# Performance work log

Hardware: AMD Instinct MI355X
Metric: run time of the kernel (lower is better)

Reference implementation:

```python
import jax, jax.numpy as jnp
import numpy as np

BLOCK = 16  # NVFP4 block size (one fp8e4m3 scale per 16 elements)
FP4_LEVELS = jnp.array([0.0, 0.5, 1.0, 1.5, 2.0, 3.0, 4.0, 6.0], dtype=jnp.float32)  # e2m1 magnitudes
FP4_MIDS = jnp.array([0.25, 0.75, 1.25, 1.75, 2.5, 3.5, 5.0], dtype=jnp.float32)     # round-to-nearest midpoints
FP8_MIN = 2.0 ** -9   # smallest positive fp8e4m3 subnormal (guards div-by-zero after scale cast)
FP8_MAX = 448.0


def fp8_e4m3_round(x):
    """Emulate casting positive float32 values to fp8 e4m3 (3 mantissa bits)."""
    e = jnp.clip(jnp.floor(jnp.log2(jnp.maximum(x, 1e-30))), -6.0, 8.0)  # -6 = min normal exponent
    step = jnp.exp2(e - 3.0)
    return jnp.clip(jnp.round(x / step) * step, 0.0, FP8_MAX)


def fp4_e2m1_quant(x):
    """Round-to-nearest onto the signed fp4 e2m1 grid {0,±0.5,±1,±1.5,±2,±3,±4,±6}."""
    idx = jnp.sum(jnp.abs(x)[..., None] > FP4_MIDS, axis=-1)
    return jnp.sign(x) * FP4_LEVELS[idx]


def quantize_activations(x2):
    """x2: [M, K] -> (fp4 values [M, K//16, 16], fp8 block scales [M, K//16])."""
    M, K = x2.shape
    xb = x2.reshape(M, K // BLOCK, BLOCK)
    amax = jnp.max(jnp.abs(xb), axis=-1)                      # per-16-block absmax
    s = jnp.maximum(fp8_e4m3_round(jnp.maximum(amax / 6.0, 1e-12)), FP8_MIN)
    q = fp4_e2m1_quant(xb / s[..., None])
    return q, s


def setup_inputs() -> dict:
    key = jax.random.key(0)
    k1, k2, k3 = jax.random.split(key, 3)
    in_f, out_f, tokens = 4096, 16384, 4096
    x = jax.random.normal(k1, (1, tokens, in_f), dtype=jnp.float32)
    # Build NVFP4 weights: quantize a random bf16-like weight per 16-element block.
    w = jax.random.normal(k2, (out_f, in_f), dtype=jnp.float32) * 0.02
    wb = w.reshape(out_f, in_f // BLOCK, BLOCK)
    weight_scale = jnp.maximum(fp8_e4m3_round(jnp.maximum(jnp.max(jnp.abs(wb), axis=-1) / 6.0, 1e-12)), FP8_MIN)
    weight_q = fp4_e2m1_quant(wb / weight_scale[..., None]).reshape(out_f, in_f)
    bias = jax.random.normal(k3, (out_f,), dtype=jnp.float32) * 0.01
    return {"x": x, "weight_q": weight_q, "weight_scale": weight_scale, "bias": bias}


def reference(x, weight_q, weight_scale, bias):
    orig_shape = x.shape
    K = orig_shape[-1]
    x2 = x.reshape(-1, K)                                     # [M, K]
    qa, sa = quantize_activations(x2)                          # fp4 values + fp8 block scales
    x_deq = (qa * sa[..., None]).reshape(x2.shape)             # dequantized activations
    N = weight_q.shape[0]
    w_deq = (weight_q.reshape(N, K // BLOCK, BLOCK) * weight_scale[..., None]).reshape(N, K)
    out = x2.dtype.type(0) + x_deq @ w_deq.T + bias[None, :]   # scaled_mm equivalent + bias
    return out.reshape(*orig_shape[:-1], N)
```

## Files before the change

kernel.cpp:

```cpp
#include <hip/hip_runtime.h>
#include <hip/hip_bf16.h>
#include <stdint.h>

typedef __attribute__((ext_vector_type(4))) float  f32x4;
typedef __attribute__((ext_vector_type(8))) short  bf16x8;
typedef __attribute__((ext_vector_type(8))) unsigned short u16x8;

#define MFMA16(d, x, y) d = __builtin_amdgcn_mfma_f32_16x16x32_bf16(x, y, d, 0, 0, 0)

static __device__ inline unsigned short f2bf(float f) {
    union { float f; unsigned u; } a; a.f = f;
    unsigned u = a.u;
    unsigned lsb = (u >> 16) & 1u;
    u += 0x7fffu + lsb;
    return (unsigned short)(u >> 16);
}

static __device__ inline float fp8_e4m3_round(float x) {
    union { float f; unsigned u; } a; a.f = x;
    int e = (int)((a.u >> 23) & 255u) - 127;
    e = e < -6 ? -6 : (e > 8 ? 8 : e);
    union { unsigned u; float f; } stp, inv;
    stp.u = (unsigned)(e - 3 + 127) << 23;
    inv.u = (unsigned)(3 - e + 127) << 23;
    float r = rintf(x * inv.f) * stp.f;
    return fminf(r, 448.0f);
}

static __device__ inline float fp4_level(float a) {
    return a > 2.5f ? (a > 3.5f ? (a > 5.0f ? 6.0f : 4.0f) : 3.0f)
                    : (a > 1.25f ? (a > 1.75f ? 2.0f : 1.5f)
                                 : (a > 0.75f ? 1.0f : (a > 0.25f ? 0.5f : 0.0f)));
}

__global__ void quant_x_kernel(const float* __restrict__ x, unsigned short* __restrict__ xd, int nblk) {
    int i = blockIdx.x * blockDim.x + threadIdx.x;
    if (i >= nblk) return;
    const float4* p = (const float4*)(x + (size_t)i * 16);
    float4 v0 = p[0], v1 = p[1], v2 = p[2], v3 = p[3];
    float vals[16] = { v0.x,v0.y,v0.z,v0.w, v1.x,v1.y,v1.z,v1.w,
                       v2.x,v2.y,v2.z,v2.w, v3.x,v3.y,v3.z,v3.w };
    float amax = 0.0f;
#pragma unroll
    for (int j = 0; j < 16; ++j) amax = fmaxf(amax, fabsf(vals[j]));
    float s0 = fmaxf(amax / 6.0f, 1e-12f);
    float s  = fmaxf(fp8_e4m3_round(s0), 1.0f / 512.0f);
    u16x8 o0, o1;
#pragma unroll
    for (int j = 0; j < 16; ++j) {
        float v = vals[j] / s;
        float lev = fp4_level(fabsf(v));
        float q = copysignf(lev, v);
        unsigned short b = f2bf(q * s);
        if (j < 8) o0[j] = b; else o1[j - 8] = b;
    }
    u16x8* dst = (u16x8*)(xd + (size_t)i * 16);
    dst[0] = o0; dst[1] = o1;
}

__global__ void deq_w_kernel(const float* __restrict__ wq, const float* __restrict__ wsc,
                             unsigned short* __restrict__ wd, int nblk) {
    int i = blockIdx.x * blockDim.x + threadIdx.x;
    if (i >= nblk) return;
    float s = wsc[i];
    const float4* p = (const float4*)(wq + (size_t)i * 16);
    float4 v0 = p[0], v1 = p[1], v2 = p[2], v3 = p[3];
    float vals[16] = { v0.x,v0.y,v0.z,v0.w, v1.x,v1.y,v1.z,v1.w,
                       v2.x,v2.y,v2.z,v2.w, v3.x,v3.y,v3.z,v3.w };
    u16x8 o0, o1;
#pragma unroll
    for (int j = 0; j < 16; ++j) {
        unsigned short b = f2bf(vals[j] * s);
        if (j < 8) o0[j] = b; else o1[j - 8] = b;
    }
    u16x8* dst = (u16x8*)(wd + (size_t)i * 16);
    dst[0] = o0; dst[1] = o1;
}

static __device__ __forceinline__ void stage_half(const unsigned short* g0, const unsigned short* g1,
                                                  size_t koff, char* d0) {
    __builtin_amdgcn_global_load_lds((const __attribute__((address_space(1))) void*)(g0 + koff),
                                     (__attribute__((address_space(3))) void*)d0, 16, 0, 0);
    __builtin_amdgcn_global_load_lds((const __attribute__((address_space(1))) void*)(g1 + koff),
                                     (__attribute__((address_space(3))) void*)(d0 + 1024), 16, 0, 0);
}

#define MFMA_ALL(AV, BV) {                                              \
    _Pragma("unroll")                                                   \
    for (int mf = 0; mf < 8; ++mf) {                                    \
        _Pragma("unroll")                                               \
        for (int nf = 0; nf < 4; ++nf) MFMA16(acc[mf][nf], AV[mf], BV[nf]); } }

#define READ12(AV, BV, OFF) {                                           \
    const char* _pa = lds + (OFF) + wr * 8192 + lane_off;               \
    const char* _pb = lds + 65536 + (OFF) + wc * 4096 + lane_off;       \
    _Pragma("unroll")                                                   \
    for (int i = 0; i < 8; ++i) AV[i] = *(const bf16x8*)(_pa + i * 1024); \
    _Pragma("unroll")                                                   \
    for (int i = 0; i < 4; ++i) BV[i] = *(const bf16x8*)(_pb + i * 1024); }

#define PH1(T, B) {                                                     \
    asm volatile("s_waitcnt vmcnt(4)" ::: "memory");                    \
    __builtin_amdgcn_s_barrier();                                       \
    __builtin_amdgcn_s_setprio(1);                                      \
    READ12(a2, b2, (B) * 32768 + 16384);                                \
    stage_half(gA0, gA1, (size_t)((T) + 1) * 64 + 32, ldsA_w + (1 - (B)) * 32768 + 16384); \
    stage_half(gB0, gB1, (size_t)((T) + 1) * 64 + 32, ldsB_w + (1 - (B)) * 32768 + 16384); \
    MFMA_ALL(a1, b1);                                                   \
    __builtin_amdgcn_s_setprio(0); }

#define PH2(T, B) {                                                     \
    asm volatile("s_waitcnt vmcnt(4)" ::: "memory");                    \
    __builtin_amdgcn_s_barrier();                                       \
    __builtin_amdgcn_s_setprio(1);                                      \
    READ12(a1, b1, (1 - (B)) * 32768);                                  \
    stage_half(gA0, gA1, (size_t)((T) + 2) * 64, ldsA_w + (B) * 32768); \
    stage_half(gB0, gB1, (size_t)((T) + 2) * 64, ldsB_w + (B) * 32768); \
    MFMA_ALL(a2, b2);                                                   \
    __builtin_amdgcn_s_setprio(0); }

__global__ __launch_bounds__(512, 2)
void gemm_kernel(const unsigned short* __restrict__ A, const unsigned short* __restrict__ Bw,
                 const float* __restrict__ bias, float* __restrict__ C,
                 int M, int N, int K) {
    extern __shared__ char lds[];
    const int tid  = threadIdx.x;
    const int lane = tid & 63;
    const int wid  = tid >> 6;
    const int wr   = wid >> 2;
    const int wc   = wid & 3;

    const int NXB = N >> 8, NYB = M >> 8;
    int bid = blockIdx.x;
    int bx, by;
    if (NXB == 64 && NYB == 16) {
        int xcd = bid & 7, c = bid >> 3;
        bx = xcd * 8 + (c & 7);
        by = c >> 3;
    } else { bx = bid % NXB; by = bid / NXB; }

    const int NT = K >> 6;

    int w0 = (lane & 15) * 64 + ((lane >> 4) << 4);
    const int lane_off = w0 ^ (((w0 >> 9) & 1) << 5);
    const int u   = (lane * 16) ^ (lane & 32);
    const int r_l = u >> 6;
    const int c_l = (u & 63) >> 1;

    const unsigned short* gA0 = A  + (size_t)(by * 256 + wid * 32 + r_l) * K + c_l;
    const unsigned short* gA1 = gA0 + (size_t)16 * K;
    const unsigned short* gB0 = Bw + (size_t)(bx * 256 + wid * 32 + r_l) * K + c_l;
    const unsigned short* gB1 = gB0 + (size_t)16 * K;
    char* ldsA_w = lds + wid * 2048 + lane * 16;
    char* ldsB_w = lds + 65536 + wid * 2048 + lane * 16;

    f32x4 acc[8][4];
#pragma unroll
    for (int m = 0; m < 8; ++m)
#pragma unroll
        for (int n = 0; n < 4; ++n)
#pragma unroll
            for (int j = 0; j < 4; ++j) acc[m][n][j] = 0.0f;

    bf16x8 a1[8], a2[8], b1[4], b2[4];

    stage_half(gA0, gA1, 0,  ldsA_w);
    stage_half(gB0, gB1, 0,  ldsB_w);
    stage_half(gA0, gA1, 32, ldsA_w + 16384);
    stage_half(gB0, gB1, 32, ldsB_w + 16384);
    stage_half(gA0, gA1, 64, ldsA_w + 32768);
    stage_half(gB0, gB1, 64, ldsB_w + 32768);
    asm volatile("s_waitcnt vmcnt(8)" ::: "memory");
    __builtin_amdgcn_s_barrier();
    READ12(a1, b1, 0);

    for (int t = 0; t <= NT - 4; t += 2) {
        PH1(t, 0);  PH2(t, 0);
        PH1(t + 1, 1);  PH2(t + 1, 1);
    }

    PH1(NT - 2, 0);
    {
        asm volatile("s_waitcnt vmcnt(4)" ::: "memory");
        __builtin_amdgcn_s_barrier();
        READ12(a1, b1, 32768);
        MFMA_ALL(a2, b2);
    }
    {
        asm volatile("s_waitcnt vmcnt(0)" ::: "memory");
        __builtin_amdgcn_s_barrier();
        READ12(a2, b2, 32768 + 16384);
        MFMA_ALL(a1, b1);
        MFMA_ALL(a2, b2);
    }

    const int row0 = by * 256 + wr * 128;
    const int col0 = bx * 256 + wc * 64;
#pragma unroll
    for (int nf = 0; nf < 4; ++nf) {
        int col = col0 + nf * 16 + (lane & 15);
        float bv = bias[col];
#pragma unroll
        for (int mf = 0; mf < 8; ++mf) {
#pragma unroll
            for (int j = 0; j < 4; ++j) {
                int row = row0 + mf * 16 + ((lane >> 4) << 2) + j;
                C[(size_t)row * N + col] = acc[mf][nf][j] + bv;
            }
        }
    }
}

extern "C" void kernel_launch(void* const* d_in, const int* in_sizes, int n_in,
                              void* d_out, int out_size, void* d_ws, size_t ws_size,
                              hipStream_t stream) {
    const float* x    = (const float*)d_in[0];
    const float* wq   = (const float*)d_in[1];
    const float* wsc  = (const float*)d_in[2];
    const float* bias = (const float*)d_in[3];
    float* out = (float*)d_out;

    const long N = in_sizes[3];
    const long K = (long)in_sizes[1] / N;
    const long M = (long)in_sizes[0] / K;

    size_t need = ((size_t)(M * K) + (size_t)(N * K)) * sizeof(unsigned short);
    if (ws_size < need) return;

    unsigned short* xd = (unsigned short*)d_ws;
    unsigned short* wd = xd + (size_t)M * K;

    {
        int nblk = (int)(M * K / 16);
        quant_x_kernel<<<(nblk + 255) / 256, 256, 0, stream>>>(x, xd, nblk);
    }
    {
        int nblk = (int)(N * K / 16);
        deq_w_kernel<<<(nblk + 255) / 256, 256, 0, stream>>>(wq, wsc, wd, nblk);
    }
    {
        hipFuncSetAttribute((const void*)gemm_kernel,
                            hipFuncAttributeMaxDynamicSharedMemorySize, 131072);
        int nwg = (int)((M / 256) * (N / 256));
        gemm_kernel<<<dim3(nwg), dim3(512), 131072, stream>>>(xd, wd, bias, out,
                                                              (int)M, (int)N, (int)K);
    }
}
```

Measured before the change: 545.4 us.

## Restructure GEMM main loop into four-quadrant ping-pong with interleaved staging

The K-loop is rewritten so each 64-wide K tile is handled as four sub-phases, one per accumulator quadrant. Each sub-phase reads only part of A/B from LDS, sits behind extra barriers and lgkmcnt waits, and slots the global->LDS staging of B and A between MFMA bursts. The aim is finer-grained overlap of LDS reads, global loads and MFMA work across the two waves per SIMD, using a two-buffer full-tile pipeline instead of the old half-tile one. It adds many more s_barriers per tile, which risks synchronization overhead and stalls if the waves do not alternate as intended.

```diff
diff --git a/kernel.cpp b/kernel.cpp
--- a/kernel.cpp
+++ b/kernel.cpp
@@ -85,39 +85,88 @@
                                      (__attribute__((address_space(3))) void*)(d0 + 1024), 16, 0, 0);
 }
 
-#define MFMA_ALL(AV, BV) {                                              \
-    _Pragma("unroll")                                                   \
-    for (int mf = 0; mf < 8; ++mf) {                                    \
-        _Pragma("unroll")                                               \
-        for (int nf = 0; nf < 4; ++nf) MFMA16(acc[mf][nf], AV[mf], BV[nf]); } }
-
-#define READ12(AV, BV, OFF) {                                           \
-    const char* _pa = lds + (OFF) + wr * 8192 + lane_off;               \
-    const char* _pb = lds + 65536 + (OFF) + wc * 4096 + lane_off;       \
-    _Pragma("unroll")                                                   \
-    for (int i = 0; i < 8; ++i) AV[i] = *(const bf16x8*)(_pa + i * 1024); \
-    _Pragma("unroll")                                                   \
-    for (int i = 0; i < 4; ++i) BV[i] = *(const bf16x8*)(_pb + i * 1024); }
-
-#define PH1(T, B) {                                                     \
-    asm volatile("s_waitcnt vmcnt(4)" ::: "memory");                    \
-    __builtin_amdgcn_s_barrier();                                       \
-    __builtin_amdgcn_s_setprio(1);                                      \
-    READ12(a2, b2, (B) * 32768 + 16384);                                \
-    stage_half(gA0, gA1, (size_t)((T) + 1) * 64 + 32, ldsA_w + (1 - (B)) * 32768 + 16384); \
-    stage_half(gB0, gB1, (size_t)((T) + 1) * 64 + 32, ldsB_w + (1 - (B)) * 32768 + 16384); \
-    MFMA_ALL(a1, b1);                                                   \
-    __builtin_amdgcn_s_setprio(0); }
-
-#define PH2(T, B) {                                                     \
-    asm volatile("s_waitcnt vmcnt(4)" ::: "memory");                    \
-    __builtin_amdgcn_s_barrier();                                       \
-    __builtin_amdgcn_s_setprio(1);                                      \
-    READ12(a1, b1, (1 - (B)) * 32768);                                  \
-    stage_half(gA0, gA1, (size_t)((T) + 2) * 64, ldsA_w + (B) * 32768); \
-    stage_half(gB0, gB1, (size_t)((T) + 2) * 64, ldsB_w + (B) * 32768); \
-    MFMA_ALL(a2, b2);                                                   \
-    __builtin_amdgcn_s_setprio(0); }
+#define VM8    asm volatile("s_waitcnt vmcnt(8)" ::: "memory")
+#define VM0    asm volatile("s_waitcnt vmcnt(0)" ::: "memory")
+#define VMNONE (void)0
+
+#define TILE(T, B, DOSTAGE, VMGATE) {                                   \
+    const char* pA = lds + (B) * 32768 + wr * 8192 + lane_off;          \
+    const char* pB = lds + 65536 + (B) * 32768 + wc * 4096 + lane_off;  \
+    const size_t k2 = (size_t)((T) + 2) * 64;                           \
+                            \
+    _Pragma("unroll")                                                   \
+    for (int m = 0; m < 4; ++m) {                                       \
+        a0[2*m]   = *(const bf16x8*)(pA + m * 1024);                    \
+        a0[2*m+1] = *(const bf16x8*)(pA + 16384 + m * 1024); }          \
+    _Pragma("unroll")                                                   \
+    for (int n = 0; n < 2; ++n) {                                       \
+        b0[2*n]   = *(const bf16x8*)(pB + n * 1024);                    \
+        b0[2*n+1] = *(const bf16x8*)(pB + 16384 + n * 1024); }          \
+    asm volatile("s_waitcnt lgkmcnt(8)" ::: "memory");                  \
+    __builtin_amdgcn_s_barrier();                                       \
+    asm volatile("s_waitcnt lgkmcnt(0)" ::: "memory");                  \
+    __builtin_amdgcn_sched_barrier(0);                                  \
+    __builtin_amdgcn_s_setprio(1);                                      \
+    _Pragma("unroll")                                                   \
+    for (int m = 0; m < 4; ++m)                                         \
+        _Pragma("unroll")                                               \
+        for (int n = 0; n < 2; ++n) {                                   \
+            MFMA16(acc[m][n], a0[2*m], b0[2*n]);                        \
+            MFMA16(acc[m][n], a0[2*m+1], b0[2*n+1]); }                  \
+    __builtin_amdgcn_s_setprio(0);                                      \
+    __builtin_amdgcn_s_barrier();                                       \
+                                      \
+    _Pragma("unroll")                                                   \
+    for (int n = 0; n < 2; ++n) {                                       \
+        b1[2*n]   = *(const bf16x8*)(pB + (2 + n) * 1024);              \
+        b1[2*n+1] = *(const bf16x8*)(pB + 16384 + (2 + n) * 1024); }    \
+    __builtin_amdgcn_s_barrier();                                       \
+    asm volatile("s_waitcnt lgkmcnt(0)" ::: "memory");                  \
+    __builtin_amdgcn_sched_barrier(0);                                  \
+    __builtin_amdgcn_s_setprio(1);                                      \
+    _Pragma("unroll")                                                   \
+    for (int m = 0; m < 4; ++m)                                         \
+        _Pragma("unroll")                                               \
+        for (int n = 0; n < 2; ++n) {                                   \
+            MFMA16(acc[m][2 + n], a0[2*m], b1[2*n]);                    \
+            MFMA16(acc[m][2 + n], a0[2*m+1], b1[2*n+1]); }              \
+    __builtin_amdgcn_s_setprio(0);                                      \
+    __builtin_amdgcn_s_barrier();                                       \
+                        \
+    _Pragma("unroll")                                                   \
+    for (int m = 0; m < 4; ++m) {                                       \
+        a1[2*m]   = *(const bf16x8*)(pA + (4 + m) * 1024);              \
+        a1[2*m+1] = *(const bf16x8*)(pA + 16384 + (4 + m) * 1024); }    \
+    if (DOSTAGE) {                                                      \
+        stage_half(gB0, gB1, k2,      ldsB_w + (B) * 32768);            \
+        stage_half(gB0, gB1, k2 + 32, ldsB_w + (B) * 32768 + 16384); }  \
+    __builtin_amdgcn_s_barrier();                                       \
+    asm volatile("s_waitcnt lgkmcnt(0)" ::: "memory");                  \
+    __builtin_amdgcn_sched_barrier(0);                                  \
+    __builtin_amdgcn_s_setprio(1);                                      \
+    _Pragma("unroll")                                                   \
+    for (int m = 0; m < 4; ++m)                                         \
+        _Pragma("unroll")                                               \
+        for (int n = 0; n < 2; ++n) {                                   \
+            MFMA16(acc[4 + m][2 + n], a1[2*m], b1[2*n]);                \
+            MFMA16(acc[4 + m][2 + n], a1[2*m+1], b1[2*n+1]); }          \
+    __builtin_amdgcn_s_setprio(0);                                      \
+    __builtin_amdgcn_s_barrier();                                       \
+                     \
+    if (DOSTAGE) {                                                      \
+        stage_half(gA0, gA1, k2,      ldsA_w + (B) * 32768);            \
+        stage_half(gA0, gA1, k2 + 32, ldsA_w + (B) * 32768 + 16384); }  \
+    VMGATE;                                                             \
+    __builtin_amdgcn_s_barrier();                                       \
+    __builtin_amdgcn_s_setprio(1);                                      \
+    _Pragma("unroll")                                                   \
+    for (int m = 0; m < 4; ++m)                                         \
+        _Pragma("unroll")                                               \
+        for (int n = 0; n < 2; ++n) {                                   \
+            MFMA16(acc[4 + m][n], a1[2*m], b0[2*n]);                    \
+            MFMA16(acc[4 + m][n], a1[2*m+1], b0[2*n+1]); }              \
+    __builtin_amdgcn_s_setprio(0);                                      \
+    __builtin_amdgcn_s_barrier(); }
 
 __global__ __launch_bounds__(512, 2)
 void gemm_kernel(const unsigned short* __restrict__ A, const unsigned short* __restrict__ Bw,
@@ -162,37 +211,25 @@
 #pragma unroll
             for (int j = 0; j < 4; ++j) acc[m][n][j] = 0.0f;
 
-    bf16x8 a1[8], a2[8], b1[4], b2[4];
-
-    stage_half(gA0, gA1, 0,  ldsA_w);
-    stage_half(gB0, gB1, 0,  ldsB_w);
-    stage_half(gA0, gA1, 32, ldsA_w + 16384);
-    stage_half(gB0, gB1, 32, ldsB_w + 16384);
-    stage_half(gA0, gA1, 64, ldsA_w + 32768);
-    stage_half(gB0, gB1, 64, ldsB_w + 32768);
+    bf16x8 a0[8], a1[8], b0[4], b1[4];
+
+    stage_half(gA0, gA1, 0,   ldsA_w);
+    stage_half(gA0, gA1, 32,  ldsA_w + 16384);
+    stage_half(gB0, gB1, 0,   ldsB_w);
+    stage_half(gB0, gB1, 32,  ldsB_w + 16384);
+    stage_half(gA0, gA1, 64,  ldsA_w + 32768);
+    stage_half(gA0, gA1, 96,  ldsA_w + 32768 + 16384);
+    stage_half(gB0, gB1, 64,  ldsB_w + 32768);
+    stage_half(gB0, gB1, 96,  ldsB_w + 32768 + 16384);
     asm volatile("s_waitcnt vmcnt(8)" ::: "memory");
     __builtin_amdgcn_s_barrier();
-    READ12(a1, b1, 0);
 
     for (int t = 0; t <= NT - 4; t += 2) {
-        PH1(t, 0);  PH2(t, 0);
-        PH1(t + 1, 1);  PH2(t + 1, 1);
-    }
-
-    PH1(NT - 2, 0);
-    {
-        asm volatile("s_waitcnt vmcnt(4)" ::: "memory");
-        __builtin_amdgcn_s_barrier();
-        READ12(a1, b1, 32768);
-        MFMA_ALL(a2, b2);
-    }
-    {
-        asm volatile("s_waitcnt vmcnt(0)" ::: "memory");
-        __builtin_amdgcn_s_barrier();
-        READ12(a2, b2, 32768 + 16384);
-        MFMA_ALL(a1, b1);
-        MFMA_ALL(a2, b2);
-    }
+        TILE(t,     0, 1, VM8);
+        TILE(t + 1, 1, 1, VM8);
+    }
+    TILE(NT - 2, 0, 0, VM0);
+    TILE(NT - 1, 1, 0, VMNONE);
 
     const int row0 = by * 256 + wr * 128;
     const int col0 = bx * 256 + wc * 64;
```

Result: slower. 575.5 us (+5.5%).
